# Optimization experiments

Measured on AMD Instinct MI355X. Metric: run time of the kernel, lower is better.

Reference implementation:

```python
import jax, jax.numpy as jnp
import numpy as np

B_, L, D_MODEL = 2, 2048, 1024
EXPAND, D_INNER, D_STATE, DT_RANK, D_CONV = 2, 2048, 16, 64, 4
DT_MIN, DT_MAX = 0.001, 0.1


def setup_inputs() -> dict:
    key = jax.random.key(0)
    ks = jax.random.split(key, 8)
    s = lambda fan: 1.0 / np.sqrt(fan)
    # S4D-real style init for A: A = -exp(A_log), A_log = log(1..n) repeated over d_inner
    A0 = jnp.broadcast_to(jnp.arange(1, D_STATE + 1, dtype=jnp.float32), (D_INNER, D_STATE))
    return {
        "x": jax.random.normal(ks[0], (B_, L, D_MODEL), jnp.float32),
        "W_in": jax.random.normal(ks[1], (D_MODEL, 2 * D_INNER), jnp.float32) * s(D_MODEL),
        "conv_k": jax.random.normal(ks[2], (D_CONV, D_INNER // EXPAND, D_INNER), jnp.float32) * s(D_CONV * D_INNER // EXPAND),
        "conv_b": jnp.zeros((D_INNER,), jnp.float32),
        "W_x": jax.random.normal(ks[3], (D_INNER, DT_RANK + 2 * D_STATE), jnp.float32) * s(D_INNER),
        "W_dt": jax.random.normal(ks[4], (DT_RANK, D_INNER), jnp.float32) * s(DT_RANK),
        "b_dt": jnp.zeros((D_INNER,), jnp.float32),
        "A_log": jnp.log(A0),
        "D": jnp.ones((D_INNER,), jnp.float32),
        "W_out": jax.random.normal(ks[5], (D_INNER, D_MODEL), jnp.float32) * s(D_INNER),
    }


def reference(x, W_in, conv_k, conv_b, W_x, W_dt, b_dt, A_log, D, W_out):
    # in_proj -> split into ssm branch and gating residual branch
    xz = x @ W_in                                   # (b, l, 2*d_inner)
    xs, res = jnp.split(xz, 2, axis=-1)
    # causal grouped conv1d (feature_group_count = expand)
    xc = jax.lax.conv_general_dilated(
        xs, conv_k, window_strides=(1,), padding=[(D_CONV - 1, 0)],
        dimension_numbers=("NWC", "WIO", "NWC"), feature_group_count=EXPAND,
    ) + conv_b
    u = jax.nn.silu(xc)                             # (b, l, d_inner)
    # x_proj -> delta(low-rank), B, C
    dbc = u @ W_x                                   # (b, l, dt_rank + 2n)
    dt_raw = dbc[..., :DT_RANK]
    Bm = dbc[..., DT_RANK:DT_RANK + D_STATE]        # (b, l, n)
    Cm = dbc[..., DT_RANK + D_STATE:]               # (b, l, n)
    delta = jax.nn.softplus(dt_raw @ W_dt + b_dt)   # (b, l, d_inner)
    delta = jnp.clip(delta, DT_MIN, DT_MAX)
    A = -jnp.exp(A_log)                             # (d_inner, n)
    dA = jnp.exp(delta[..., None] * A)              # (b, l, d_inner, n)
    dBu = delta[..., None] * u[..., None] * Bm[:, :, None, :]  # (b, l, d_inner, n)

    def step(h, inp):
        dA_t, dBu_t, C_t = inp                      # (b,d,n),(b,d,n),(b,n)
        h = dA_t * h + dBu_t
        y_t = jnp.einsum('bdn,bn->bd', h, C_t)
        return h, y_t

    h0 = jnp.zeros((x.shape[0], D_INNER, D_STATE), dA.dtype)
    _, y = jax.lax.scan(step, h0, (dA.transpose(1, 0, 2, 3), dBu.transpose(1, 0, 2, 3), Cm.transpose(1, 0, 2)))
    y = y.transpose(1, 0, 2) + u * D                # (b, l, d_inner)
    out = (y * jax.nn.silu(res)) @ W_out            # (b, l, d_model)
    return out
```

## Files before the change

kernel.cpp:

```cpp
#include <hip/hip_runtime.h>
#include <math.h>


typedef unsigned short ushort_t;
typedef unsigned int uint_t;
typedef __bf16 bf16x8 __attribute__((ext_vector_type(8)));
typedef float floatx4 __attribute__((ext_vector_type(4)));

#define LDS_STRIDE 40

__device__ __forceinline__ float silu_f(float x) { return x / (1.0f + __expf(-x)); }

__device__ __forceinline__ unsigned short f2bf(float f) {
    unsigned u = __float_as_uint(f);
    unsigned r = u + 0x7fffu + ((u >> 16) & 1u);
    return (unsigned short)(r >> 16);
}
__device__ __forceinline__ float bf2f(unsigned short h) {
    return __uint_as_float(((unsigned)h) << 16);
}
__device__ __forceinline__ uint_t packhl(float v) {
    const unsigned short h = f2bf(v);
    const unsigned short l = f2bf(v - bf2f(h));
    return (uint_t)h | ((uint_t)l << 16);
}
__device__ __forceinline__ float unpack_sum(uint_t pk) {
    return __uint_as_float(pk << 16) + __uint_as_float(pk & 0xffff0000u);
}
__device__ __forceinline__ void unpack8(uint4 w0, uint4 w1, uint4& H, uint4& L) {
    H.x = (w0.x & 0xffffu) | (w0.y << 16);  L.x = (w0.x >> 16) | (w0.y & 0xffff0000u);
    H.y = (w0.z & 0xffffu) | (w0.w << 16);  L.y = (w0.z >> 16) | (w0.w & 0xffff0000u);
    H.z = (w1.x & 0xffffu) | (w1.y << 16);  L.z = (w1.x >> 16) | (w1.y & 0xffff0000u);
    H.w = (w1.z & 0xffffu) | (w1.w << 16);  L.w = (w1.z >> 16) | (w1.w & 0xffff0000u);
}
__device__ __forceinline__ size_t faddr(int n, int k, int KC) {
    return ((size_t)((n >> 4) * KC + (k >> 5)) * 64 + (n & 15) + (((k >> 3) & 3) << 4)) * 8
           + (k & 7);
}

__global__ __launch_bounds__(256) void prep_all(
    const float* __restrict__ x, const float* __restrict__ W_in,
    const float* __restrict__ conv_k, const float* __restrict__ W_out,
    const float* __restrict__ W_x,
    uint_t* __restrict__ xpk,
    ushort_t* __restrict__ WinF, ushort_t* __restrict__ convkF,
    ushort_t* __restrict__ WoutF, ushort_t* __restrict__ WxF,
    ushort_t* __restrict__ XSP_h)
{
    __shared__ float ts[32][33];
    const int bid = blockIdx.x;
    const int t = threadIdx.x;
    if (bid < 4096) {
        const size_t i4 = ((size_t)bid * 256 + t) * 4;
        float4 v = *(const float4*)&x[i4];
        uint4 pk;
        pk.x = packhl(v.x); pk.y = packhl(v.y); pk.z = packhl(v.z); pk.w = packhl(v.w);
        *(uint4*)&xpk[i4] = pk;
        return;
    }
    if (bid >= 18432 && bid < 19456) {
        const int idx = (bid - 18432) * 256 + t;
        const int r = idx >> 11, k = idx & 2047;
        float v = (r < 96) ? W_x[(size_t)k * 96 + r] : 0.f;
        WxF[faddr(r, k, 64)] = f2bf(v);
        return;
    }
    if (bid >= 19456) {
        const int idx = (bid - 19456) * 256 + t;
        const int b = idx / 6144, rem = idx % 6144;
        const int lp = rem >> 11, c = rem & 2047;
        XSP_h[((size_t)b * 2051 + lp) * 2048 + c] = 0;
        return;
    }
    const float* src; int R, C, KC; ushort_t* dst; int bx, by;
    if (bid < 8192)       { src = W_in;   R = 1024; C = 4096; KC = 32;  dst = WinF;
                            int l = bid - 4096;  bx = l & 127; by = l >> 7; }
    else if (bid < 16384) { src = conv_k; R = 4096; C = 2048; KC = 128; dst = convkF;
                            int l = bid - 8192;  bx = l & 63;  by = l >> 6; }
    else                  { src = W_out;  R = 2048; C = 1024; KC = 64;  dst = WoutF;
                            int l = bid - 16384; bx = l & 31;  by = l >> 5; }
    const int tx = t & 31, ty = t >> 5;
    const int r0 = by * 32, c0 = bx * 32;
    #pragma unroll
    for (int j = 0; j < 4; ++j)
        ts[ty + j * 8][tx] = src[(size_t)(r0 + ty + j * 8) * C + c0 + tx];
    __syncthreads();
    #pragma unroll
    for (int j = 0; j < 4; ++j) {
        const int n = c0 + ty + j * 8, k = r0 + tx;
        dst[faddr(n, k, KC)] = f2bf(ts[tx][ty + j * 8]);
    }
}

template<int MODE>
__global__ __launch_bounds__(256) void gemm2(
    const uint_t* __restrict__ Apk, const ushort_t* __restrict__ Bf, int Kfull,
    float* __restrict__ Cf, ushort_t* __restrict__ Oh)
{
    __shared__ __align__(16) ushort_t As_h[128 * LDS_STRIDE];
    __shared__ __align__(16) ushort_t As_l[128 * LDS_STRIDE];
    const int t = threadIdx.x;
    int bx, by;
    if (MODE == 2) { bx = blockIdx.x; by = blockIdx.y; }
    else {
        const int lin = blockIdx.x, xcd = lin & 7, s = lin >> 3;
        bx = s >> 2;
        by = xcd * 4 + (s & 3);
    }
    const int m0 = by * 128;
    const int n0 = (MODE == 2) ? 0 : bx * 128;
    const int kbeg = (MODE == 2) ? bx * 512 : 0;
    const int kend = (MODE == 2) ? kbeg + 512 : Kfull;
    const int KC = Kfull >> 5;
    const int lane = t & 63, wave = t >> 6;
    const int wm = (wave >> 1) * 64, wn = (wave & 1) * 64;
    const int m16 = lane & 15, q = lane >> 4;
    const int n16b = (n0 + wn) >> 4;
    const int r_0 = t >> 2, cc_0 = (t & 3) * 8;
    const int r_1 = (t + 256) >> 2, cc_1 = ((t + 256) & 3) * 8;

    uint4 a00 = *(const uint4*)&Apk[(size_t)(m0 + r_0) * Kfull + kbeg + cc_0];
    uint4 a01 = *(const uint4*)&Apk[(size_t)(m0 + r_0) * Kfull + kbeg + cc_0 + 4];
    uint4 a10 = *(const uint4*)&Apk[(size_t)(m0 + r_1) * Kfull + kbeg + cc_1];
    uint4 a11 = *(const uint4*)&Apk[(size_t)(m0 + r_1) * Kfull + kbeg + cc_1 + 4];
    bf16x8 bc[4];
    {
        const int kc = kbeg >> 5;
        #pragma unroll
        for (int j = 0; j < 4; ++j)
            bc[j] = *(const bf16x8*)&Bf[(((size_t)(n16b + j) * KC + kc) * 64 + lane) * 8];
    }

    floatx4 acc[4][4];
    const floatx4 zz = {0.f, 0.f, 0.f, 0.f};
    #pragma unroll
    for (int i = 0; i < 4; ++i)
        #pragma unroll
        for (int j = 0; j < 4; ++j) acc[i][j] = zz;

    for (int k0 = kbeg; k0 < kend; k0 += 32) {
        uint4 H, L;
        unpack8(a00, a01, H, L);
        *(uint4*)&As_h[r_0 * LDS_STRIDE + cc_0] = H;
        *(uint4*)&As_l[r_0 * LDS_STRIDE + cc_0] = L;
        unpack8(a10, a11, H, L);
        *(uint4*)&As_h[r_1 * LDS_STRIDE + cc_1] = H;
        *(uint4*)&As_l[r_1 * LDS_STRIDE + cc_1] = L;
        __syncthreads();
        bf16x8 bn[4];
        if (k0 + 32 < kend) {
            const int kn = k0 + 32, kc = kn >> 5;
            a00 = *(const uint4*)&Apk[(size_t)(m0 + r_0) * Kfull + kn + cc_0];
            a01 = *(const uint4*)&Apk[(size_t)(m0 + r_0) * Kfull + kn + cc_0 + 4];
            a10 = *(const uint4*)&Apk[(size_t)(m0 + r_1) * Kfull + kn + cc_1];
            a11 = *(const uint4*)&Apk[(size_t)(m0 + r_1) * Kfull + kn + cc_1 + 4];
            #pragma unroll
            for (int j = 0; j < 4; ++j)
                bn[j] = *(const bf16x8*)&Bf[(((size_t)(n16b + j) * KC + kc) * 64 + lane) * 8];
        }
        bf16x8 ah[4], al[4];
        #pragma unroll
        for (int i = 0; i < 4; ++i) {
            const int off = (wm + i * 16 + m16) * LDS_STRIDE + q * 8;
            ah[i] = *(const bf16x8*)&As_h[off];
            al[i] = *(const bf16x8*)&As_l[off];
        }
        #pragma unroll
        for (int i = 0; i < 4; ++i)
            #pragma unroll
            for (int j = 0; j < 4; ++j) {
                acc[i][j] = __builtin_amdgcn_mfma_f32_16x16x32_bf16(ah[i], bc[j], acc[i][j], 0, 0, 0);
                acc[i][j] = __builtin_amdgcn_mfma_f32_16x16x32_bf16(al[i], bc[j], acc[i][j], 0, 0, 0);
            }
        #pragma unroll
        for (int j = 0; j < 4; ++j) bc[j] = bn[j];
        __syncthreads();
    }

    float* Cp = (MODE == 2) ? (Cf + (size_t)bx * 393216) : Cf;
    #pragma unroll
    for (int i = 0; i < 4; ++i) {
        const int row_b = m0 + wm + i * 16 + q * 4;
        #pragma unroll
        for (int j = 0; j < 4; ++j) {
            const int col = n0 + wn + j * 16 + m16;
            #pragma unroll
            for (int rr = 0; rr < 4; ++rr) {
                const int row = row_b + rr;
                const float v = acc[i][j][rr];
                if (MODE == 0) {
                    if (n0 < 2048) {
                        const int b = row >> 11, l = row & 2047;
                        Oh[((size_t)b * 2051 + l + 3) * 2048 + col] = f2bf(v);
                    } else {
                        Cp[(size_t)row * 2048 + (col - 2048)] = v;
                    }
                } else if (MODE == 1) {
                    Cp[(size_t)row * 1024 + col] = v;
                } else {
                    if (col < 96) Cp[(size_t)row * 96 + col] = v;
                }
            }
        }
    }
}

__global__ __launch_bounds__(256) void conv2(
    const ushort_t* __restrict__ Xh, const ushort_t* __restrict__ Bf,
    const float* __restrict__ bias, uint_t* __restrict__ Upk)
{
    __shared__ __align__(16) ushort_t As_h[128 * LDS_STRIDE];
    const int t = threadIdx.x;
    const int lin = blockIdx.x, xcd = lin & 7, s = lin >> 3;
    const int sweep = s >> 5, r = s & 31;
    const int bxp = r >> 1;
    const int by = xcd * 4 + ((sweep << 1) | (r & 1));
    const int m0 = by * 128, n0 = bxp * 128;
    const int g1024 = (n0 >= 1024) ? 1024 : 0;
    const int lane = t & 63, wave = t >> 6;
    const int wm = (wave >> 1) * 64, wn = (wave & 1) * 64;
    const int m16 = lane & 15, q = lane >> 4;
    const int n16b = (n0 + wn) >> 4;
    const int r_0 = t >> 2, cc_0 = (t & 3) * 8;
    const int r_1 = (t + 256) >> 2, cc_1 = ((t + 256) & 3) * 8;
    const int p_0 = m0 + r_0, b_0 = p_0 >> 11, l_0 = p_0 & 2047;
    const int p_1 = m0 + r_1, b_1 = p_1 >> 11, l_1 = p_1 & 2047;

    auto aA = [&](int bb, int ll, int k0, int cc) -> size_t {
        const int w = k0 >> 10;
        const int i = (k0 & 1023) + cc;
        return ((size_t)bb * 2051 + ll + w) * 2048 + g1024 + i;
    };

    uint4 pa0 = *(const uint4*)&Xh[aA(b_0, l_0, 0, cc_0)];
    uint4 pa1 = *(const uint4*)&Xh[aA(b_1, l_1, 0, cc_1)];
    bf16x8 bc[4];
    #pragma unroll
    for (int j = 0; j < 4; ++j)
        bc[j] = *(const bf16x8*)&Bf[(((size_t)(n16b + j) * 128 + 0) * 64 + lane) * 8];

    floatx4 acc[4][4];
    const floatx4 zz = {0.f, 0.f, 0.f, 0.f};
    #pragma unroll
    for (int i = 0; i < 4; ++i)
        #pragma unroll
        for (int j = 0; j < 4; ++j) acc[i][j] = zz;

    for (int k0 = 0; k0 < 4096; k0 += 32) {
        *(uint4*)&As_h[r_0 * LDS_STRIDE + cc_0] = pa0;
        *(uint4*)&As_h[r_1 * LDS_STRIDE + cc_1] = pa1;
        __syncthreads();
        bf16x8 bn[4];
        if (k0 + 32 < 4096) {
            const int kn = k0 + 32, kc = kn >> 5;
            pa0 = *(const uint4*)&Xh[aA(b_0, l_0, kn, cc_0)];
            pa1 = *(const uint4*)&Xh[aA(b_1, l_1, kn, cc_1)];
            #pragma unroll
            for (int j = 0; j < 4; ++j)
                bn[j] = *(const bf16x8*)&Bf[(((size_t)(n16b + j) * 128 + kc) * 64 + lane) * 8];
        }
        bf16x8 ah[4];
        #pragma unroll
        for (int i = 0; i < 4; ++i)
            ah[i] = *(const bf16x8*)&As_h[(wm + i * 16 + m16) * LDS_STRIDE + q * 8];
        #pragma unroll
        for (int i = 0; i < 4; ++i)
            #pragma unroll
            for (int j = 0; j < 4; ++j)
                acc[i][j] = __builtin_amdgcn_mfma_f32_16x16x32_bf16(ah[i], bc[j], acc[i][j], 0, 0, 0);
        #pragma unroll
        for (int j = 0; j < 4; ++j) bc[j] = bn[j];
        __syncthreads();
    }

    #pragma unroll
    for (int i = 0; i < 4; ++i) {
        const int row_b = m0 + wm + i * 16 + q * 4;
        #pragma unroll
        for (int j = 0; j < 4; ++j) {
            const int col = n0 + wn + j * 16 + m16;
            const float bz = bias[col];
            #pragma unroll
            for (int rr = 0; rr < 4; ++rr) {
                const int row = row_b + rr;
                const float v = silu_f(acc[i][j][rr] + bz);
                Upk[(size_t)row * 2048 + col] = packhl(v);
            }
        }
    }
}

__global__ __launch_bounds__(256) void dbc_reduce(
    const float* __restrict__ DBCP, float* __restrict__ DBC)
{
    const int i = blockIdx.x * 256 + threadIdx.x;
    DBC[i] = (DBCP[i] + DBCP[393216 + i]) + (DBCP[786432 + i] + DBCP[1179648 + i]);
}

__global__ __launch_bounds__(256) void delta_kernel(
    const float* __restrict__ DBC, const float* __restrict__ W_dt,
    const float* __restrict__ b_dt, float* __restrict__ DELTA)
{
    const int n  = blockIdx.x * 256 + threadIdx.x;
    const int p0 = blockIdx.y * 16;
    const int t  = threadIdx.x;
    __shared__ float dt_s[16][64];
    #pragma unroll
    for (int j = 0; j < 4; ++j) {
        const int lin = j * 256 + t;
        const int r = lin >> 6, k = lin & 63;
        dt_s[r][k] = DBC[(size_t)(p0 + r) * 96 + k];
    }
    __syncthreads();
    float acc[16];
    const float bz = b_dt[n];
    #pragma unroll
    for (int r = 0; r < 16; ++r) acc[r] = bz;
    for (int k = 0; k < 64; ++k) {
        const float wv = W_dt[(size_t)k * 2048 + n];
        #pragma unroll
        for (int r = 0; r < 16; ++r) acc[r] += dt_s[r][k] * wv;
    }
    #pragma unroll
    for (int r = 0; r < 16; ++r) {
        float a = acc[r];
        float sp = (a > 20.f) ? a : log1pf(expf(a));
        sp = fminf(fmaxf(sp, 0.001f), 0.1f);
        DELTA[(size_t)(p0 + r) * 2048 + n] = sp;
    }
}

__global__ __launch_bounds__(256) void scan_p1(
    const float* __restrict__ DELTA, const uint_t* __restrict__ Upk,
    const float* __restrict__ DBC, const float* __restrict__ A_log,
    float* __restrict__ HEND, float* __restrict__ SD)
{
    const int t = threadIdx.x;
    const int d = blockIdx.x * 256 + t;
    const int c = blockIdx.y;
    const int b = blockIdx.z;
    const int p0 = b * 2048 + c * 32;
    __shared__ float Bs[32][16];
    for (int lin = t; lin < 512; lin += 256) {
        const int s = lin >> 4, n = lin & 15;
        Bs[s][n] = DBC[(size_t)(p0 + s) * 96 + 64 + n];
    }
    __syncthreads();
    float Af[16];
    *(float4*)&Af[0]  = *(const float4*)&A_log[(size_t)d * 16 + 0];
    *(float4*)&Af[4]  = *(const float4*)&A_log[(size_t)d * 16 + 4];
    *(float4*)&Af[8]  = *(const float4*)&A_log[(size_t)d * 16 + 8];
    *(float4*)&Af[12] = *(const float4*)&A_log[(size_t)d * 16 + 12];
    #pragma unroll
    for (int n = 0; n < 16; ++n) Af[n] = -__expf(Af[n]);

    float h[16] = {};
    float sd = 0.f;
    for (int s = 0; s < 32; ++s) {
        const size_t ix = (size_t)(p0 + s) * 2048 + d;
        const float dv = DELTA[ix];
        const float uv = unpack_sum(Upk[ix]);
        const float du = dv * uv;
        sd += dv;
        #pragma unroll
        for (int n = 0; n < 16; ++n)
            h[n] = __expf(dv * Af[n]) * h[n] + du * Bs[s][n];
    }
    const size_t hb = (((size_t)c * 2 + b) * 2048 + d) * 16;
    *(float4*)&HEND[hb + 0]  = *(float4*)&h[0];
    *(float4*)&HEND[hb + 4]  = *(float4*)&h[4];
    *(float4*)&HEND[hb + 8]  = *(float4*)&h[8];
    *(float4*)&HEND[hb + 12] = *(float4*)&h[12];
    SD[((size_t)c * 2 + b) * 2048 + d] = sd;
}

__global__ __launch_bounds__(256) void scan_p2(
    const float* __restrict__ HEND, const float* __restrict__ SD,
    const float* __restrict__ A_log, float* __restrict__ HINIT)
{
    const int g = blockIdx.x * 256 + threadIdx.x;
    const int n = g & 15, d = (g >> 4) & 2047, b = (g >> 15) & 1;
    const float Af = -__expf(A_log[(size_t)d * 16 + n]);
    float h = 0.f;
    #pragma unroll 8
    for (int c = 0; c < 64; ++c) {
        const size_t cb = (size_t)c * 2 + b;
        const size_t idx = (cb * 2048 + d) * 16 + n;
        HINIT[idx] = h;
        h = __expf(Af * SD[cb * 2048 + d]) * h + HEND[idx];
    }
}

__global__ __launch_bounds__(256) void scan_p3(
    const float* __restrict__ DELTA, const uint_t* __restrict__ Upk,
    const float* __restrict__ DBC, const float* __restrict__ RES,
    const float* __restrict__ A_log, const float* __restrict__ Dp,
    const float* __restrict__ HINIT, uint_t* __restrict__ Gpk)
{
    const int t = threadIdx.x;
    const int d = blockIdx.x * 256 + t;
    const int c = blockIdx.y;
    const int b = blockIdx.z;
    const int p0 = b * 2048 + c * 32;
    __shared__ float Bs[32][16];
    __shared__ float Cs[32][16];
    for (int lin = t; lin < 512; lin += 256) {
        const int s = lin >> 4, n = lin & 15;
        Bs[s][n] = DBC[(size_t)(p0 + s) * 96 + 64 + n];
        Cs[s][n] = DBC[(size_t)(p0 + s) * 96 + 80 + n];
    }
    __syncthreads();
    float Af[16];
    *(float4*)&Af[0]  = *(const float4*)&A_log[(size_t)d * 16 + 0];
    *(float4*)&Af[4]  = *(const float4*)&A_log[(size_t)d * 16 + 4];
    *(float4*)&Af[8]  = *(const float4*)&A_log[(size_t)d * 16 + 8];
    *(float4*)&Af[12] = *(const float4*)&A_log[(size_t)d * 16 + 12];
    #pragma unroll
    for (int n = 0; n < 16; ++n) Af[n] = -__expf(Af[n]);

    const size_t hb = (((size_t)c * 2 + b) * 2048 + d) * 16;
    float h[16];
    *(float4*)&h[0]  = *(const float4*)&HINIT[hb + 0];
    *(float4*)&h[4]  = *(const float4*)&HINIT[hb + 4];
    *(float4*)&h[8]  = *(const float4*)&HINIT[hb + 8];
    *(float4*)&h[12] = *(const float4*)&HINIT[hb + 12];
    const float Dd = Dp[d];

    for (int s = 0; s < 32; ++s) {
        const int p = p0 + s;
        const size_t ix = (size_t)p * 2048 + d;
        const float dv = DELTA[ix];
        const float uv = unpack_sum(Upk[ix]);
        const float du = dv * uv;
        float y = 0.f;
        #pragma unroll
        for (int n = 0; n < 16; ++n) {
            h[n] = __expf(dv * Af[n]) * h[n] + du * Bs[s][n];
            y += h[n] * Cs[s][n];
        }
        const float resv = RES[ix];
        const float gv = (y + uv * Dd) * silu_f(resv);
        Gpk[ix] = packhl(gv);
    }
}

extern "C" void kernel_launch(void* const* d_in, const int* in_sizes, int n_in,
                              void* d_out, int out_size, void* d_ws, size_t ws_size,
                              hipStream_t stream) {
    const float* x      = (const float*)d_in[0];
    const float* W_in   = (const float*)d_in[1];
    const float* conv_k = (const float*)d_in[2];
    const float* conv_b = (const float*)d_in[3];
    const float* W_x    = (const float*)d_in[4];
    const float* W_dt   = (const float*)d_in[5];
    const float* b_dt   = (const float*)d_in[6];
    const float* A_log  = (const float*)d_in[7];
    const float* Dv     = (const float*)d_in[8];
    const float* W_out  = (const float*)d_in[9];
    float* out = (float*)d_out;

    char* base = (char*)d_ws;
    float*    RES      = (float*)(base);
    uint_t*   Upk      = (uint_t*)(base + 33554432);
    float*    DELTA    = (float*)(base + 67108864);
    ushort_t* XSP_h    = (ushort_t*)(base + 100663296);
    float*    HEND     = (float*)(base + 100663296);
    uint_t*   xpk      = (uint_t*)(base + 117465088);
    ushort_t* convkF   = (ushort_t*)(base + 134242304);
    uint_t*   Gpk      = (uint_t*)(base + 117465088);
    ushort_t* WinF     = (ushort_t*)(base + 151019520);
    ushort_t* WoutF    = (ushort_t*)(base + 159408128);
    ushort_t* WxF      = (ushort_t*)(base + 163602432);
    float*    DBCP     = (float*)(base + 164126720);
    float*    DBC      = (float*)(base + 170418176);
    float*    SD       = (float*)(base + 171991040);
    float*    HINIT    = (float*)(base + 173039616);

    prep_all<<<19504, 256, 0, stream>>>(x, W_in, conv_k, W_out, W_x,
                                        xpk, WinF, convkF, WoutF, WxF, XSP_h);
    gemm2<0><<<1024, 256, 0, stream>>>(xpk, WinF, 1024, RES, XSP_h);
    conv2<<<512, 256, 0, stream>>>(XSP_h, convkF, conv_b, Upk);
    gemm2<2><<<dim3(4, 32), 256, 0, stream>>>(Upk, WxF, 2048, DBCP, nullptr);
    dbc_reduce<<<1536, 256, 0, stream>>>(DBCP, DBC);
    delta_kernel<<<dim3(8, 256), 256, 0, stream>>>(DBC, W_dt, b_dt, DELTA);
    scan_p1<<<dim3(8, 64, 2), 256, 0, stream>>>(DELTA, Upk, DBC, A_log, HEND, SD);
    scan_p2<<<256, 256, 0, stream>>>(HEND, SD, A_log, HINIT);
    scan_p3<<<dim3(8, 64, 2), 256, 0, stream>>>(DELTA, Upk, DBC, RES, A_log, Dv,
                                                HINIT, Gpk);
    gemm2<1><<<256, 256, 0, stream>>>(Gpk, WoutF, 2048, out, nullptr);
}
```

Before: 506.5 us.

## Pipeline conv GEMM with direct global-to-LDS loads, double buffering and swizzle

```diff
diff --git a/kernel.cpp b/kernel.cpp
--- a/kernel.cpp
+++ b/kernel.cpp
@@ -8,6 +8,10 @@
 typedef float floatx4 __attribute__((ext_vector_type(4)));
 
 #define LDS_STRIDE 40
+
+#define GLOAD16(gp, lp) \
+    __builtin_amdgcn_global_load_lds((const __attribute__((address_space(1))) void*)(gp), \
+                                     (__attribute__((address_space(3))) void*)(lp), 16, 0, 0)
 
 __device__ __forceinline__ float silu_f(float x) { return x / (1.0f + __expf(-x)); }
 
@@ -205,11 +209,12 @@
     }
 }
 
-__global__ __launch_bounds__(256) void conv2(
+__global__ __launch_bounds__(256, 2) void conv2(
     const ushort_t* __restrict__ Xh, const ushort_t* __restrict__ Bf,
     const float* __restrict__ bias, uint_t* __restrict__ Upk)
 {
-    __shared__ __align__(16) ushort_t As_h[128 * LDS_STRIDE];
+    __shared__ __align__(16) ushort_t Asw[2][128 * 64];
+    __shared__ __align__(16) ushort_t Bsw[2][16 * 512];
     const int t = threadIdx.x;
     const int lin = blockIdx.x, xcd = lin & 7, s = lin >> 3;
     const int sweep = s >> 5, r = s & 31;
@@ -220,24 +225,29 @@
     const int lane = t & 63, wave = t >> 6;
     const int wm = (wave >> 1) * 64, wn = (wave & 1) * 64;
     const int m16 = lane & 15, q = lane >> 4;
-    const int n16b = (n0 + wn) >> 4;
-    const int r_0 = t >> 2, cc_0 = (t & 3) * 8;
-    const int r_1 = (t + 256) >> 2, cc_1 = ((t + 256) & 3) * 8;
-    const int p_0 = m0 + r_0, b_0 = p_0 >> 11, l_0 = p_0 & 2047;
-    const int p_1 = m0 + r_1, b_1 = p_1 >> 11, l_1 = p_1 & 2047;
-
-    auto aA = [&](int bb, int ll, int k0, int cc) -> size_t {
-        const int w = k0 >> 10;
-        const int i = (k0 & 1023) + cc;
-        return ((size_t)bb * 2051 + ll + w) * 2048 + g1024 + i;
+    const int l8 = lane >> 3, c8 = lane & 7;
+    const int cs = c8 ^ l8;
+    const int n16base = n0 >> 4;
+    const int Xrow0 = (m0 >> 11) * 2051 + (m0 & 2047);
+
+    auto stage = [&](int dbuf, int ph, int Tn) {
+        const int wtap = Tn >> 4;
+        const int i0 = (Tn << 6) & 1023;
+        const int kc = Tn * 2 + ph;
+        #pragma unroll
+        for (int ii = 0; ii < 2; ++ii) {
+            const int rr0 = ph * 64 + wave * 16 + ii * 8;
+            const size_t gidx = (size_t)(Xrow0 + rr0 + l8 + wtap) * 2048
+                              + g1024 + i0 + cs * 8;
+            GLOAD16(Xh + gidx, &Asw[dbuf][rr0 * 64]);
+        }
+        #pragma unroll
+        for (int jj = 0; jj < 2; ++jj) {
+            const int jn = wave * 2 + jj;
+            const size_t gidx = ((size_t)(n16base + jn) * 128 + kc) * 512 + lane * 8;
+            GLOAD16(Bf + gidx, &Bsw[dbuf][(ph * 8 + jn) * 512]);
+        }
     };
-
-    uint4 pa0 = *(const uint4*)&Xh[aA(b_0, l_0, 0, cc_0)];
-    uint4 pa1 = *(const uint4*)&Xh[aA(b_1, l_1, 0, cc_1)];
-    bf16x8 bc[4];
-    #pragma unroll
-    for (int j = 0; j < 4; ++j)
-        bc[j] = *(const bf16x8*)&Bf[(((size_t)(n16b + j) * 128 + 0) * 64 + lane) * 8];
 
     floatx4 acc[4][4];
     const floatx4 zz = {0.f, 0.f, 0.f, 0.f};
@@ -246,31 +256,51 @@
         #pragma unroll
         for (int j = 0; j < 4; ++j) acc[i][j] = zz;
 
-    for (int k0 = 0; k0 < 4096; k0 += 32) {
-        *(uint4*)&As_h[r_0 * LDS_STRIDE + cc_0] = pa0;
-        *(uint4*)&As_h[r_1 * LDS_STRIDE + cc_1] = pa1;
-        __syncthreads();
-        bf16x8 bn[4];
-        if (k0 + 32 < 4096) {
-            const int kn = k0 + 32, kc = kn >> 5;
-            pa0 = *(const uint4*)&Xh[aA(b_0, l_0, kn, cc_0)];
-            pa1 = *(const uint4*)&Xh[aA(b_1, l_1, kn, cc_1)];
+    auto phase = [&](int dbuf, int kcL) {
+        bf16x8 ah[4], bb[4];
+        #pragma unroll
+        for (int mi = 0; mi < 4; ++mi) {
+            const int rr2 = wm + mi * 16 + m16;
+            const int ch = ((kcL << 2) | q) ^ (m16 & 7);
+            ah[mi] = *(const bf16x8*)&Asw[dbuf][rr2 * 64 + ch * 8];
+        }
+        #pragma unroll
+        for (int j = 0; j < 4; ++j) {
+            const int ss = (kcL << 3) + (wn >> 4) + j;
+            bb[j] = *(const bf16x8*)&Bsw[dbuf][ss * 512 + lane * 8];
+        }
+        __builtin_amdgcn_s_setprio(1);
+        #pragma unroll
+        for (int mi = 0; mi < 4; ++mi)
             #pragma unroll
             for (int j = 0; j < 4; ++j)
-                bn[j] = *(const bf16x8*)&Bf[(((size_t)(n16b + j) * 128 + kc) * 64 + lane) * 8];
-        }
-        bf16x8 ah[4];
-        #pragma unroll
-        for (int i = 0; i < 4; ++i)
-            ah[i] = *(const bf16x8*)&As_h[(wm + i * 16 + m16) * LDS_STRIDE + q * 8];
-        #pragma unroll
-        for (int i = 0; i < 4; ++i)
-            #pragma unroll
-            for (int j = 0; j < 4; ++j)
-                acc[i][j] = __builtin_amdgcn_mfma_f32_16x16x32_bf16(ah[i], bc[j], acc[i][j], 0, 0, 0);
-        #pragma unroll
-        for (int j = 0; j < 4; ++j) bc[j] = bn[j];
-        __syncthreads();
+                acc[mi][j] = __builtin_amdgcn_mfma_f32_16x16x32_bf16(ah[mi], bb[j], acc[mi][j], 0, 0, 0);
+        __builtin_amdgcn_s_setprio(0);
+    };
+
+    stage(0, 0, 0);
+    stage(0, 1, 0);
+
+    int cur = 0;
+    for (int T = 0; T < 64; ++T) {
+        if (T < 63) {
+            stage(cur ^ 1, 0, T + 1);
+            asm volatile("s_waitcnt vmcnt(4)" ::: "memory");
+        } else {
+            asm volatile("s_waitcnt vmcnt(0)" ::: "memory");
+        }
+        __builtin_amdgcn_s_barrier();
+        asm volatile("" ::: "memory");
+        phase(cur, 0);
+        asm volatile("" ::: "memory");
+        __builtin_amdgcn_s_barrier();
+        asm volatile("" ::: "memory");
+        if (T < 63) stage(cur ^ 1, 1, T + 1);
+        phase(cur, 1);
+        asm volatile("" ::: "memory");
+        __builtin_amdgcn_s_barrier();
+        asm volatile("" ::: "memory");
+        cur ^= 1;
     }
 
     #pragma unroll
```

Result: slower. 517.2 us (+2.1%).
